# Optimization experiments

Hardware: AMD Instinct MI355X
Metric: run time of the kernel (lower is better)

The kernel has to match this reference:

```python
import jax, jax.numpy as jnp
import numpy as np

MAX_DISP = 60
MIN_DISP = 1
BLOCK = 9
EPS = 1e-6


def _box_sum(x, k):
    # sum over all channels and a k x k window, 'same' padding -> [B,1,H,W]
    C = x.shape[1]
    f = jnp.ones((1, C, k, k), x.dtype)
    return jax.lax.conv_general_dilated(
        x, f, window_strides=(1, 1), padding=[(k // 2, k // 2)] * 2,
        dimension_numbers=('NCHW', 'OIHW', 'NCHW'))


def _forward(imageL, imageR):
    B, C, H, W = imageL.shape
    n = BLOCK * BLOCK * C  # box-window element count (over channels)
    col = jnp.arange(W)

    # precomputed box statistics (computed once, reused for every disparity)
    LSum = _box_sum(imageL, BLOCK); LAve = LSum / n; LAve2 = LAve ** 2
    L2Sum = _box_sum(imageL ** 2, BLOCK)
    RSum = _box_sum(imageR, BLOCK); RAve = RSum / n; RAve2 = RAve ** 2
    R2Sum = _box_sum(imageR ** 2, BLOCK)

    sqrtL = jnp.sqrt(L2Sum - 2 * LAve * LSum + n * LAve2 + 1e-5)
    sqrtR = jnp.sqrt(R2Sum - 2 * RAve * RSum + n * RAve2 + 1e-5)

    def shift_r(a, i):  # shift right by i columns, zero-fill on the left (== narrow + pad in torch)
        idx = jnp.maximum(col - i, 0)
        return jnp.where(col >= i, a[..., idx], jnp.zeros((), a.dtype))

    def shift_l(a, i):  # shift left by i columns, zero-fill on the right
        idx = jnp.minimum(col + i, W - 1)
        return jnp.where(col < W - i, a[..., idx], jnp.zeros((), a.dtype))

    def corrL(i):
        sR = shift_r(imageR, i)
        sRSum = shift_r(RSum, i)
        sR2Sum = shift_r(R2Sum, i)
        sRAve = shift_r(RAve, i)
        sRAve2 = shift_r(RAve2, i)
        prod = _box_sum(imageL * sR, BLOCK) - LAve * sRSum - sRAve * LSum + n * LAve * sRAve
        sqrtS = jnp.sqrt(sR2Sum - 2 * sRAve * sRSum + n * sRAve2 + 1e-5)
        c = (prod + EPS) / (sqrtL * sqrtS + EPS)
        return jnp.where(col >= i, c, 0.0)  # corrL[:, :, :, :i] = 0

    def corrR(i):
        sL = shift_l(imageL, i)
        sLSum = shift_l(LSum, i)
        sL2Sum = shift_l(L2Sum, i)
        sLAve = shift_l(LAve, i)
        sLAve2 = shift_l(LAve2, i)
        prod = _box_sum(imageR * sL, BLOCK) - RAve * sLSum - sLAve * RSum + n * RAve * sLAve
        sqrtS = jnp.sqrt(sL2Sum - 2 * sLAve * sLSum + n * sLAve2 + 1e-5)
        c = (prod + EPS) / (sqrtR * sqrtS + EPS)
        return jnp.where(col < W - i, c, 0.0)  # corrR[:, :, :, W-i:] = 0

    disps = jnp.arange(MIN_DISP, MAX_DISP + 1)  # D = maxDisp - minDisp + 1 levels
    costL = jax.vmap(corrL)(disps)  # [D,B,1,H,W]
    costR = jax.vmap(corrR)(disps)  # [D,B,1,H,W]
    return jnp.stack([costL, costR])  # [2,D,B,1,H,W]


def setup_inputs() -> dict:
    key = jax.random.key(0)
    k1, k2 = jax.random.split(key)
    imageL = jax.random.uniform(k1, (1, 3, 540, 960), jnp.float32)
    imageR = jax.random.uniform(k2, (1, 3, 540, 960), jnp.float32)
    return {
        'imageL': imageL,
        'imageR': imageR,
        'f': jnp.ones((1,), jnp.float32),
        'blDis': jnp.ones((1,), jnp.float32),
        'beta': jnp.ones((1,), jnp.float32),
    }


def reference(imageL, imageR, f, blDis, beta):
    # f / blDis / beta are accepted by the original signature but unused in the
    # reachable computation (beta only appears in the broken CostToDisp stub).
    return _forward(imageL, imageR)
```

## Files before the change

### kernel.cpp

```cpp
#include <hip/hip_runtime.h>

#define HH 540
#define WW 960
#define NC 3
#define ND 60
#define NP (HH * WW)
#define STRIP 45
#define OUTC 248

__global__ __launch_bounds__(256) void k_stats_h(
    const float* __restrict__ L, const float* __restrict__ R,
    float* __restrict__ hsL, float* __restrict__ hsLL,
    float* __restrict__ hsR, float* __restrict__ hsRR) {
    int x = blockIdx.x * blockDim.x + threadIdx.x;
    int y = blockIdx.y;
    if (x >= WW) return;
    float a = 0.f, a2 = 0.f, b = 0.f, b2 = 0.f;
#pragma unroll
    for (int dx = -4; dx <= 4; ++dx) {
        int xx = x + dx;
        if (xx < 0 || xx >= WW) continue;
#pragma unroll
        for (int c = 0; c < NC; ++c) {
            float l = L[(c * HH + y) * WW + xx];
            float r = R[(c * HH + y) * WW + xx];
            a += l; a2 = fmaf(l, l, a2);
            b += r; b2 = fmaf(r, r, b2);
        }
    }
    int o = y * WW + x;
    hsL[o] = a; hsLL[o] = a2; hsR[o] = b; hsRR[o] = b2;
}

__global__ __launch_bounds__(256) void k_stats_v(
    const float* __restrict__ hsL, const float* __restrict__ hsLL,
    const float* __restrict__ hsR, const float* __restrict__ hsRR,
    float* __restrict__ LSum, float* __restrict__ sqLa,
    float* __restrict__ RSn, float* __restrict__ sqRa) {
    int x = blockIdx.x * blockDim.x + threadIdx.x;
    int y = blockIdx.y;
    if (x >= WW) return;
    float a = 0.f, a2 = 0.f, b = 0.f, b2 = 0.f;
#pragma unroll
    for (int dy = -4; dy <= 4; ++dy) {
        int yy = y + dy;
        if (yy < 0 || yy >= HH) continue;
        int o = yy * WW + x;
        a += hsL[o]; a2 += hsLL[o]; b += hsR[o]; b2 += hsRR[o];
    }
    const float inv_n = 1.0f / 243.0f;
    int o = y * WW + x;
    LSum[o] = a;
    sqLa[o] = sqrtf(fmaf(-a * inv_n, a, a2) + 1e-5f);
    RSn[o]  = b * inv_n;
    sqRa[o] = sqrtf(fmaf(-b * inv_n, b, b2) + 1e-5f);
}

__device__ __forceinline__ float qval(const float* __restrict__ L,
                                      const float* __restrict__ R,
                                      int yy, int xq, int d) {
    if ((unsigned)yy >= (unsigned)HH) return 0.f;
    int o = yy * WW + xq;
    float q = L[o] * R[o - d];
    q = fmaf(L[o + NP], R[o - d + NP], q);
    q = fmaf(L[o + 2 * NP], R[o - d + 2 * NP], q);
    return q;
}

__global__ __launch_bounds__(256) void k_cost(
    const float* __restrict__ L, const float* __restrict__ R,
    const float* __restrict__ LSum, const float* __restrict__ sqLa,
    const float* __restrict__ RSn, const float* __restrict__ sqRa,
    float* __restrict__ out) {
    __shared__ float vbuf[256];
    const int t  = threadIdx.x;
    const int d  = blockIdx.z + 1;
    const int y0 = blockIdx.y * STRIP;
    const int x0 = blockIdx.x * OUTC;
    const int xq = x0 - 4 + t;

    const bool qvalid = (xq >= d) && (xq < WW);

    float v = 0.f;
    if (qvalid) {
#pragma unroll
        for (int dy = -4; dy <= 4; ++dy) v += qval(L, R, y0 + dy, xq, d);
    }

    float* outL = out + (size_t)(d - 1) * NP;
    float* outR = out + (size_t)ND * NP + (size_t)(d - 1) * NP;
    const bool isOut = (t >= 4) && (t < 4 + OUTC) && (xq < WW);

    for (int y = y0; y < y0 + STRIP; ++y) {
        vbuf[t] = v;
        __syncthreads();
        if (isOut) {
            float cross = 0.f;
#pragma unroll
            for (int j = -4; j <= 4; ++j) cross += vbuf[t + j];
            const int x = xq;
            const int o = y * WW + x;
            float cl = 0.f;
            if (x >= d) {
                float num = fmaf(-LSum[o], RSn[o - d], cross) + 1e-6f;
                float den = fmaf(sqLa[o], sqRa[o - d], 1e-6f);
                cl = num * __builtin_amdgcn_rcpf(den);
                outR[o - d] = cl;
            }
            outL[o] = cl;
            if (x >= WW - d) outR[o] = 0.f;
        }
        __syncthreads();
        if (qvalid) {
            v += qval(L, R, y + 5, xq, d) - qval(L, R, y - 4, xq, d);
        }
    }
}

extern "C" void kernel_launch(void* const* d_in, const int* in_sizes, int n_in,
                              void* d_out, int out_size, void* d_ws, size_t ws_size,
                              hipStream_t stream) {
    const float* L = (const float*)d_in[0];
    const float* R = (const float*)d_in[1];
    float* out = (float*)d_out;
    float* ws = (float*)d_ws;

    float* hsL  = ws + 0 * (size_t)NP;
    float* hsLL = ws + 1 * (size_t)NP;
    float* hsR  = ws + 2 * (size_t)NP;
    float* hsRR = ws + 3 * (size_t)NP;
    float* LSum = ws + 4 * (size_t)NP;
    float* sqLa = ws + 5 * (size_t)NP;
    float* RSn  = ws + 6 * (size_t)NP;
    float* sqRa = ws + 7 * (size_t)NP;

    dim3 blk(256);
    dim3 g1((WW + 255) / 256, HH);
    k_stats_h<<<g1, blk, 0, stream>>>(L, R, hsL, hsLL, hsR, hsRR);
    k_stats_v<<<g1, blk, 0, stream>>>(hsL, hsLL, hsR, hsRR, LSum, sqLa, RSn, sqRa);

    dim3 g3((WW + OUTC - 1) / OUTC, HH / STRIP, ND);
    k_cost<<<g3, blk, 0, stream>>>(L, R, LSum, sqLa, RSn, sqRa, out);
}
```

Before: 374.1 us.

## Process six disparities per block with shared R row staging and vectorized output

Each cost block now handles six consecutive disparities instead of one. The needed R rows are staged in shared memory and the L loads are shared across those disparities, which cuts redundant global reads of L and R. The horizontal box sum moves to a sliding window in which each thread produces 8 consecutive outputs, with float4 reads of LSum/sqLa and float4 writes of the left cost. The exchange is more shared memory, more registers, and fewer blocks in the grid.

Measured after the change: 517.3 us. 38.3% more time.

```diff
diff --git a/kernel.cpp b/kernel.cpp
--- a/kernel.cpp
+++ b/kernel.cpp
@@ -7,6 +7,12 @@
 #define NP (HH * WW)
 #define STRIP 45
 #define OUTC 248
+#define DT 6
+#define NDT (ND / DT)
+#define RBW 264
+#define VBW 260
+#define GRP 31
+#define P2T (DT * GRP)
 
 __global__ __launch_bounds__(256) void k_stats_h(
     const float* __restrict__ L, const float* __restrict__ R,
@@ -56,64 +62,159 @@
     sqRa[o] = sqrtf(fmaf(-b * inv_n, b, b2) + 1e-5f);
 }
 
-__device__ __forceinline__ float qval(const float* __restrict__ L,
-                                      const float* __restrict__ R,
-                                      int yy, int xq, int d) {
-    if ((unsigned)yy >= (unsigned)HH) return 0.f;
-    int o = yy * WW + xq;
-    float q = L[o] * R[o - d];
-    q = fmaf(L[o + NP], R[o - d + NP], q);
-    q = fmaf(L[o + 2 * NP], R[o - d + 2 * NP], q);
-    return q;
-}
-
 __global__ __launch_bounds__(256) void k_cost(
     const float* __restrict__ L, const float* __restrict__ R,
     const float* __restrict__ LSum, const float* __restrict__ sqLa,
     const float* __restrict__ RSn, const float* __restrict__ sqRa,
     float* __restrict__ out) {
-    __shared__ float vbuf[256];
-    const int t  = threadIdx.x;
-    const int d  = blockIdx.z + 1;
-    const int y0 = blockIdx.y * STRIP;
-    const int x0 = blockIdx.x * OUTC;
-    const int xq = x0 - 4 + t;
-
-    const bool qvalid = (xq >= d) && (xq < WW);
-
-    float v = 0.f;
-    if (qvalid) {
-#pragma unroll
-        for (int dy = -4; dy <= 4; ++dy) v += qval(L, R, y0 + dy, xq, d);
-    }
-
-    float* outL = out + (size_t)(d - 1) * NP;
-    float* outR = out + (size_t)ND * NP + (size_t)(d - 1) * NP;
-    const bool isOut = (t >= 4) && (t < 4 + OUTC) && (xq < WW);
+    __shared__ __align__(16) float rb[2][NC][RBW];
+    __shared__ __align__(16) float vbuf[DT * VBW];
+
+    const int t   = threadIdx.x;
+    const int y0  = blockIdx.y * STRIP;
+    const int x0  = blockIdx.x * OUTC;
+    const int dlo = blockIdx.z * DT + 1;
+    const int xq  = x0 - 4 + t;
+    const int rbase = x0 - dlo - 9;
+    const bool xok = ((unsigned)xq < WW);
+
+    float v[DT];
+#pragma unroll
+    for (int k = 0; k < DT; ++k) v[k] = 0.f;
+
+    const int d_k = (t < P2T) ? (t / GRP) : (DT - 1);
+    const int g   = t - ((t < P2T) ? d_k * GRP : t);
+    const bool p2 = (t < P2T);
+    const int X   = x0 + 8 * ((t < P2T) ? (t - d_k * GRP) : 0);
+    const int d   = dlo + d_k;
+    float* const outLp = out + (size_t)(d - 1) * NP;
+    float* const outRp = outLp + (size_t)ND * NP;
+    (void)g;
+
+    auto stageR = [&](int slot, int row) {
+#pragma unroll
+        for (int ch = 0; ch < NC; ++ch) {
+            int gc = rbase + t;
+            gc = max(0, min(WW - 1, gc));
+            rb[slot][ch][t] = R[(ch * HH + row) * WW + gc];
+            if (t < RBW - 256) {
+                int gc2 = rbase + t + 256;
+                gc2 = max(0, min(WW - 1, gc2));
+                rb[slot][ch][t + 256] = R[(ch * HH + row) * WW + gc2];
+            }
+        }
+    };
+    auto loadL = [&](int row, float* l) {
+#pragma unroll
+        for (int ch = 0; ch < NC; ++ch)
+            l[ch] = xok ? L[(ch * HH + row) * WW + xq] : 0.f;
+    };
+
+    for (int r = y0 - 4; r <= y0 + 4; ++r) {
+        const bool rv = ((unsigned)r < HH);
+        float l[NC] = {0.f, 0.f, 0.f};
+        if (rv) { stageR(0, r); loadL(r, l); }
+        __syncthreads();
+        if (rv && xok) {
+#pragma unroll
+            for (int k = 0; k < DT; ++k) {
+                if (xq >= dlo + k) {
+                    const int ri = t + 5 - k;
+                    float q = l[0] * rb[0][0][ri];
+                    q = fmaf(l[1], rb[0][1][ri], q);
+                    q = fmaf(l[2], rb[0][2][ri], q);
+                    v[k] += q;
+                }
+            }
+        }
+        __syncthreads();
+    }
 
     for (int y = y0; y < y0 + STRIP; ++y) {
-        vbuf[t] = v;
-        __syncthreads();
-        if (isOut) {
-            float cross = 0.f;
-#pragma unroll
-            for (int j = -4; j <= 4; ++j) cross += vbuf[t + j];
-            const int x = xq;
-            const int o = y * WW + x;
-            float cl = 0.f;
-            if (x >= d) {
-                float num = fmaf(-LSum[o], RSn[o - d], cross) + 1e-6f;
-                float den = fmaf(sqLa[o], sqRa[o - d], 1e-6f);
-                cl = num * __builtin_amdgcn_rcpf(den);
-                outR[o - d] = cl;
-            }
-            outL[o] = cl;
-            if (x >= WW - d) outR[o] = 0.f;
-        }
-        __syncthreads();
-        if (qvalid) {
-            v += qval(L, R, y + 5, xq, d) - qval(L, R, y - 4, xq, d);
-        }
+        const int rA = y + 5, rS = y - 4;
+        const bool vA = ((unsigned)rA < HH), vS = ((unsigned)rS < HH);
+        float lA[NC] = {0.f, 0.f, 0.f}, lS[NC] = {0.f, 0.f, 0.f};
+        if (vA) { stageR(0, rA); loadL(rA, lA); }
+        if (vS) { stageR(1, rS); loadL(rS, lS); }
+#pragma unroll
+        for (int k = 0; k < DT; ++k) vbuf[k * VBW + t] = v[k];
+        __syncthreads();
+
+        if (p2 && X < WW) {
+            const float4* vb = (const float4*)&vbuf[d_k * VBW + (X - x0)];
+            float4 w0 = vb[0], w1 = vb[1], w2 = vb[2], w3 = vb[3];
+            const float q0 = w0.x, q1 = w0.y, q2 = w0.z, q3 = w0.w;
+            const float q4 = w1.x, q5 = w1.y, q6 = w1.z, q7 = w1.w;
+            const float q8 = w2.x, q9 = w2.y, q10 = w2.z, q11 = w2.w;
+            const float q12 = w3.x, q13 = w3.y, q14 = w3.z, q15 = w3.w;
+            float s[8];
+            s[0] = ((q0 + q1) + (q2 + q3)) + ((q4 + q5) + (q6 + q7)) + q8;
+            s[1] = s[0] + q9  - q0;
+            s[2] = s[1] + q10 - q1;
+            s[3] = s[2] + q11 - q2;
+            s[4] = s[3] + q12 - q3;
+            s[5] = s[4] + q13 - q4;
+            s[6] = s[5] + q14 - q5;
+            s[7] = s[6] + q15 - q6;
+
+            const int o = y * WW + X;
+            float4 lsA = *(const float4*)&LSum[o];
+            float4 lsB = *(const float4*)&LSum[o + 4];
+            float4 slA = *(const float4*)&sqLa[o];
+            float4 slB = *(const float4*)&sqLa[o + 4];
+            const float ls[8] = {lsA.x, lsA.y, lsA.z, lsA.w, lsB.x, lsB.y, lsB.z, lsB.w};
+            const float sl[8] = {slA.x, slA.y, slA.z, slA.w, slB.x, slB.y, slB.z, slB.w};
+
+            if (X >= d && (X + 7) < (WW - d)) {
+                float cl[8];
+#pragma unroll
+                for (int j = 0; j < 8; ++j) {
+                    const int od = o + j - d;
+                    float num = fmaf(-ls[j], RSn[od], s[j]) + 1e-6f;
+                    float den = fmaf(sl[j], sqRa[od], 1e-6f);
+                    cl[j] = num * __builtin_amdgcn_rcpf(den);
+                    outRp[od] = cl[j];
+                }
+                *(float4*)&outLp[o]     = make_float4(cl[0], cl[1], cl[2], cl[3]);
+                *(float4*)&outLp[o + 4] = make_float4(cl[4], cl[5], cl[6], cl[7]);
+            } else {
+#pragma unroll
+                for (int j = 0; j < 8; ++j) {
+                    const int x = X + j;
+                    float cl = 0.f;
+                    if (x >= d) {
+                        const int od = o + j - d;
+                        float num = fmaf(-ls[j], RSn[od], s[j]) + 1e-6f;
+                        float den = fmaf(sl[j], sqRa[od], 1e-6f);
+                        cl = num * __builtin_amdgcn_rcpf(den);
+                        outRp[od] = cl;
+                    }
+                    outLp[o + j] = cl;
+                    if (x >= WW - d) outRp[o + j] = 0.f;
+                }
+            }
+        }
+
+        if (xok) {
+#pragma unroll
+            for (int k = 0; k < DT; ++k) {
+                const int ri = t + 5 - k;
+                const bool qv = (xq >= dlo + k);
+                float qa = 0.f, qs = 0.f;
+                if (vA && qv) {
+                    qa = lA[0] * rb[0][0][ri];
+                    qa = fmaf(lA[1], rb[0][1][ri], qa);
+                    qa = fmaf(lA[2], rb[0][2][ri], qa);
+                }
+                if (vS && qv) {
+                    qs = lS[0] * rb[1][0][ri];
+                    qs = fmaf(lS[1], rb[1][1][ri], qs);
+                    qs = fmaf(lS[2], rb[1][2][ri], qs);
+                }
+                v[k] += qa - qs;
+            }
+        }
+        __syncthreads();
     }
 }
 
@@ -139,6 +240,6 @@
     k_stats_h<<<g1, blk, 0, stream>>>(L, R, hsL, hsLL, hsR, hsRR);
     k_stats_v<<<g1, blk, 0, stream>>>(hsL, hsLL, hsR, hsRR, LSum, sqLa, RSn, sqRa);
 
-    dim3 g3((WW + OUTC - 1) / OUTC, HH / STRIP, ND);
+    dim3 g3((WW + OUTC - 1) / OUTC, HH / STRIP, NDT);
     k_cost<<<g3, blk, 0, stream>>>(L, R, LSum, sqLa, RSn, sqRa, out);
 }
```

## Split cost kernel into vertical box-sum pass and vectorized horizontal pass

Applied to the files above, without the earlier changes.

Replaces the fused per-disparity cost kernel, which used shared memory and two barriers per row, with two kernels. The first computes vertical 9-row sums of the channel products with a register ring buffer and writes them to a 60-plane workspace. The second does the horizontal 9-tap sum with float4 loads, four pixels per thread, and writes both cost volumes. This removes the per-row synchronisation, but adds a full write and read of about 124 MB of intermediate data through global memory.

Measured after the change: 470.4 us. 1.26x slower.

```diff
diff --git a/kernel.cpp b/kernel.cpp
--- a/kernel.cpp
+++ b/kernel.cpp
@@ -5,8 +5,9 @@
 #define NC 3
 #define ND 60
 #define NP (HH * WW)
-#define STRIP 45
-#define OUTC 248
+#define XT 256
+#define YS 90
+#define RY 4
 
 __global__ __launch_bounds__(256) void k_stats_h(
     const float* __restrict__ L, const float* __restrict__ R,
@@ -56,63 +57,110 @@
     sqRa[o] = sqrtf(fmaf(-b * inv_n, b, b2) + 1e-5f);
 }
 
-__device__ __forceinline__ float qval(const float* __restrict__ L,
-                                      const float* __restrict__ R,
-                                      int yy, int xq, int d) {
-    if ((unsigned)yy >= (unsigned)HH) return 0.f;
-    int o = yy * WW + xq;
-    float q = L[o] * R[o - d];
-    q = fmaf(L[o + NP], R[o - d + NP], q);
-    q = fmaf(L[o + 2 * NP], R[o - d + 2 * NP], q);
-    return q;
+__global__ __launch_bounds__(256) void k_vq(
+    const float* __restrict__ L, const float* __restrict__ R,
+    float* __restrict__ vq) {
+    const int t  = threadIdx.x;
+    const int x  = blockIdx.x * XT + t;
+    const int y0 = blockIdx.y * YS;
+    const int d  = blockIdx.z + 1;
+    if (x >= WW) return;
+    float* const vqd = vq + (size_t)blockIdx.z * NP;
+
+    if (x < d) {
+        for (int y = y0; y < y0 + YS; ++y) vqd[y * WW + x] = 0.f;
+        return;
+    }
+    const float* const Lx = L + x;
+    const float* const Rx = R + (x - d);
+    auto pval = [&](int row) -> float {
+        if ((unsigned)row >= (unsigned)HH) return 0.f;
+        const int o = row * WW;
+        float q = Lx[o] * Rx[o];
+        q = fmaf(Lx[o + NP],     Rx[o + NP],     q);
+        q = fmaf(Lx[o + 2 * NP], Rx[o + 2 * NP], q);
+        return q;
+    };
+
+    float ring[9];
+    float S = 0.f;
+#pragma unroll
+    for (int j = 0; j < 9; ++j) {
+        float p = pval(y0 - 4 + j);
+        ring[(j + 5) % 9] = p;
+        S += p;
+    }
+    for (int yb = 0; yb < YS; yb += 9) {
+#pragma unroll
+        for (int j = 0; j < 9; ++j) {
+            const int y = y0 + yb + j;
+            vqd[y * WW + x] = S;
+            const float pnew = pval(y + 5);
+            const int slot = (j + 5) % 9;
+            S += pnew - ring[slot];
+            ring[slot] = pnew;
+        }
+    }
 }
 
-__global__ __launch_bounds__(256) void k_cost(
-    const float* __restrict__ L, const float* __restrict__ R,
+__global__ __launch_bounds__(256) void k_cost_h(
+    const float* __restrict__ vq,
     const float* __restrict__ LSum, const float* __restrict__ sqLa,
     const float* __restrict__ RSn, const float* __restrict__ sqRa,
     float* __restrict__ out) {
-    __shared__ float vbuf[256];
-    const int t  = threadIdx.x;
-    const int d  = blockIdx.z + 1;
-    const int y0 = blockIdx.y * STRIP;
-    const int x0 = blockIdx.x * OUTC;
-    const int xq = x0 - 4 + t;
+    const int t = threadIdx.x;
+    const int X = 4 * t;
+    if (X >= WW) return;
+    const int d  = blockIdx.y + 1;
+    const int y0 = blockIdx.x * RY;
+    const float* const vqd = vq + (size_t)blockIdx.y * NP;
+    float* const outLp = out + (size_t)blockIdx.y * NP;
+    float* const outRp = outLp + (size_t)ND * NP;
+    const float4 z4 = make_float4(0.f, 0.f, 0.f, 0.f);
 
-    const bool qvalid = (xq >= d) && (xq < WW);
+    for (int y = y0; y < y0 + RY; ++y) {
+        const int o = y * WW + X;
+        const float4 w0 = (t > 0)   ? *(const float4*)&vqd[o - 4] : z4;
+        const float4 w1 = *(const float4*)&vqd[o];
+        const float4 w2 = (X + 4 < WW) ? *(const float4*)&vqd[o + 4] : z4;
+        const float s0 = ((w0.x + w0.y) + (w0.z + w0.w))
+                       + ((w1.x + w1.y) + (w1.z + w1.w)) + w2.x;
+        const float s1 = s0 + w2.y - w0.x;
+        const float s2 = s1 + w2.z - w0.y;
+        const float s3 = s2 + w2.w - w0.z;
+        const float s[4] = {s0, s1, s2, s3};
 
-    float v = 0.f;
-    if (qvalid) {
+        const float4 ls = *(const float4*)&LSum[o];
+        const float4 sl = *(const float4*)&sqLa[o];
+        const float lsa[4] = {ls.x, ls.y, ls.z, ls.w};
+        const float sla[4] = {sl.x, sl.y, sl.z, sl.w};
+
+        if (X >= d && X + 3 < WW - d) {
+            const int od = o - d;
+            float cl[4];
 #pragma unroll
-        for (int dy = -4; dy <= 4; ++dy) v += qval(L, R, y0 + dy, xq, d);
-    }
-
-    float* outL = out + (size_t)(d - 1) * NP;
-    float* outR = out + (size_t)ND * NP + (size_t)(d - 1) * NP;
-    const bool isOut = (t >= 4) && (t < 4 + OUTC) && (xq < WW);
-
-    for (int y = y0; y < y0 + STRIP; ++y) {
-        vbuf[t] = v;
-        __syncthreads();
-        if (isOut) {
-            float cross = 0.f;
+            for (int j = 0; j < 4; ++j) {
+                const float num = fmaf(-lsa[j], RSn[od + j], s[j]) + 1e-6f;
+                const float den = fmaf(sla[j], sqRa[od + j], 1e-6f);
+                cl[j] = num * __builtin_amdgcn_rcpf(den);
+                outRp[od + j] = cl[j];
+            }
+            *(float4*)&outLp[o] = make_float4(cl[0], cl[1], cl[2], cl[3]);
+        } else {
 #pragma unroll
-            for (int j = -4; j <= 4; ++j) cross += vbuf[t + j];
-            const int x = xq;
-            const int o = y * WW + x;
-            float cl = 0.f;
-            if (x >= d) {
-                float num = fmaf(-LSum[o], RSn[o - d], cross) + 1e-6f;
-                float den = fmaf(sqLa[o], sqRa[o - d], 1e-6f);
-                cl = num * __builtin_amdgcn_rcpf(den);
-                outR[o - d] = cl;
+            for (int j = 0; j < 4; ++j) {
+                const int x = X + j;
+                float cl = 0.f;
+                if (x >= d) {
+                    const int od = o + j - d;
+                    const float num = fmaf(-lsa[j], RSn[od], s[j]) + 1e-6f;
+                    const float den = fmaf(sla[j], sqRa[od], 1e-6f);
+                    cl = num * __builtin_amdgcn_rcpf(den);
+                    outRp[od] = cl;
+                }
+                outLp[o + j] = cl;
+                if (x >= WW - d) outRp[o + j] = 0.f;
             }
-            outL[o] = cl;
-            if (x >= WW - d) outR[o] = 0.f;
-        }
-        __syncthreads();
-        if (qvalid) {
-            v += qval(L, R, y + 5, xq, d) - qval(L, R, y - 4, xq, d);
         }
     }
 }
@@ -133,12 +181,16 @@
     float* sqLa = ws + 5 * (size_t)NP;
     float* RSn  = ws + 6 * (size_t)NP;
     float* sqRa = ws + 7 * (size_t)NP;
+    float* vq   = ws + 8 * (size_t)NP;
 
     dim3 blk(256);
     dim3 g1((WW + 255) / 256, HH);
     k_stats_h<<<g1, blk, 0, stream>>>(L, R, hsL, hsLL, hsR, hsRR);
     k_stats_v<<<g1, blk, 0, stream>>>(hsL, hsLL, hsR, hsRR, LSum, sqLa, RSn, sqRa);
 
-    dim3 g3((WW + OUTC - 1) / OUTC, HH / STRIP, ND);
-    k_cost<<<g3, blk, 0, stream>>>(L, R, LSum, sqLa, RSn, sqRa, out);
+    dim3 g2((WW + XT - 1) / XT, HH / YS, ND);
+    k_vq<<<g2, blk, 0, stream>>>(L, R, vq);
+
+    dim3 g3(HH / RY, ND);
+    k_cost_h<<<g3, blk, 0, stream>>>(vq, LSum, sqLa, RSn, sqRa, out);
 }
```
